# Performance work log

Measured on AMD Instinct MI355X. Metric: run time of the kernel, lower is better.

## Reference

```python
import jax, jax.numpy as jnp
import numpy as np

NUM_NODES = 100000
NUM_EDGES = 50000
NUM_CONN = 800000
IN_DIM = 256
HIDDEN = 128
EDGE_ATTR_DIM = 17
LN_EPS = 1e-5


def setup_inputs() -> dict:
    key = jax.random.key(0)
    k1, k2, k3, kw1, kb1, kg, kbeta, kw2, kb2 = jax.random.split(key, 9)
    node_features = jax.random.normal(k1, (NUM_NODES, IN_DIM), dtype=jnp.float32)
    nodes = jax.random.randint(k2, (NUM_CONN,), 0, NUM_NODES, dtype=jnp.int64)
    edges = jax.random.randint(k3, (NUM_CONN,), 0, NUM_EDGES, dtype=jnp.int64)
    hyperedge_index = jnp.stack([nodes, edges], axis=0)
    # MLP params (Linear(in,hid) -> LayerNorm -> ReLU -> Dropout(eval:identity) -> Linear(hid,out))
    W1 = jax.random.normal(kw1, (IN_DIM, HIDDEN), dtype=jnp.float32) * (1.0 / np.sqrt(IN_DIM))
    b1 = jax.random.normal(kb1, (HIDDEN,), dtype=jnp.float32) * 0.01
    ln_g = jnp.ones((HIDDEN,), dtype=jnp.float32)
    ln_b = jnp.zeros((HIDDEN,), dtype=jnp.float32)
    W2 = jax.random.normal(kw2, (HIDDEN, EDGE_ATTR_DIM), dtype=jnp.float32) * (1.0 / np.sqrt(HIDDEN))
    b2 = jax.random.normal(kb2, (EDGE_ATTR_DIM,), dtype=jnp.float32) * 0.01
    return {"node_features": node_features, "hyperedge_index": hyperedge_index,
            "W1": W1, "b1": b1, "ln_g": ln_g, "ln_b": ln_b, "W2": W2, "b2": b2}


def reference(node_features, hyperedge_index, W1, b1, ln_g, ln_b, W2, b2):
    nodes = hyperedge_index[0]
    edges = hyperedge_index[1]
    # indices are in-range by construction (torch valid_mask is all-True here)
    gathered = node_features[nodes]                         # [num_conn, in_dim]
    summed = jax.ops.segment_sum(gathered, edges, num_segments=NUM_EDGES)
    counts = jax.ops.segment_sum(jnp.ones(edges.shape, node_features.dtype), edges,
                                 num_segments=NUM_EDGES)
    edge_features = summed / jnp.clip(counts, 1.0)[:, None]  # mean aggregation
    # decoder MLP (dropout inactive in eval)
    h = edge_features @ W1 + b1
    mu = jnp.mean(h, axis=-1, keepdims=True)
    var = jnp.mean(jnp.square(h - mu), axis=-1, keepdims=True)
    h = (h - mu) * jax.lax.rsqrt(var + LN_EPS) * ln_g + ln_b
    h = jax.nn.relu(h)
    return h @ W2 + b2                                      # [num_edges, edge_attr_dim]
```

## Files before the change

kernel.cpp:

```cpp
#include <hip/hip_runtime.h>
#include <hip/hip_bf16.h>
#include <stdint.h>

#define NUM_NODES 100000
#define NUM_EDGES 50000
#define NUM_CONN  800000
#define IN_DIM    256
#define HIDDEN    128
#define EDGE_DIM  17
#define PAD       64
#define CSTRIDE   16

typedef __bf16 bf16x8 __attribute__((ext_vector_type(8)));
typedef float  f32x4  __attribute__((ext_vector_type(4)));


__global__ void prep_kernel(const float* __restrict__ W1, const float* __restrict__ W2,
                            __bf16* __restrict__ w1f, __bf16* __restrict__ w2f,
                            int* __restrict__ counts2) {
    int i = blockIdx.x * 256 + threadIdx.x;
    if (i < NUM_EDGES) {
        int4 z = {0, 0, 0, 0};
        int4* c4 = (int4*)(counts2 + (size_t)i * CSTRIDE);
        c4[0] = z; c4[1] = z; c4[2] = z; c4[3] = z;
    }
    if (i < 4096) {
        int lane = i & 63, t = (i >> 6) & 7, kc2 = i >> 9;
        int m = lane & 15, q = lane >> 4;
        int n = t * 16 + m;
        int kbase = kc2 * 32 + q * 8;
        __bf16* dst = w1f + (size_t)i * 8;
        #pragma unroll
        for (int ki = 0; ki < 8; ++ki)
            dst[ki] = (__bf16)W1[(size_t)(kbase + ki) * HIDDEN + n];
    } else if (i < 4608) {
        int f = i - 4096;
        int lane = f & 63, t = (f >> 6) & 1, ks = f >> 7;
        int m = lane & 15, q = lane >> 4;
        int n = t * 16 + m;
        int kbase = ks * 32 + q * 8;
        __bf16* dst = w2f + (size_t)f * 8;
        #pragma unroll
        for (int ki = 0; ki < 8; ++ki)
            dst[ki] = (n < EDGE_DIM) ? (__bf16)W2[(size_t)(kbase + ki) * EDGE_DIM + n]
                                     : (__bf16)0.0f;
    }
}

#define FRONT_BLOCKS 2346
__global__ __launch_bounds__(256, 4) void front_kernel(const int* __restrict__ idx,
        int stride, int* __restrict__ counts2, int* __restrict__ slots,
        const float* __restrict__ nf, const __bf16* __restrict__ w1f,
        __bf16* __restrict__ pbf) {
    __shared__ __align__(16) __bf16 lds_w[16384];
    const int nb = blockIdx.x / 3, r3 = blockIdx.x % 3;
    if (r3 == 1) {
        long c0 = ((long)nb * 256 + threadIdx.x) * 4;
        if (c0 < NUM_CONN) {
            int nd[4], ed[4];
            if (stride == 2) {
                #pragma unroll
                for (int k = 0; k < 2; ++k) {
                    int4 vn = ((const int4*)idx)[c0 / 2 + k];
                    int4 ve = ((const int4*)(idx + 2 * NUM_CONN))[c0 / 2 + k];
                    nd[2 * k] = vn.x; nd[2 * k + 1] = vn.z;
                    ed[2 * k] = ve.x; ed[2 * k + 1] = ve.z;
                }
            } else {
                #pragma unroll
                for (int k = 0; k < 4; ++k) {
                    nd[k] = idx[c0 + k];
                    ed[k] = idx[NUM_CONN + c0 + k];
                }
            }
            int pos[4];
            #pragma unroll
            for (int k = 0; k < 4; ++k)
                pos[k] = atomicAdd(&counts2[(size_t)ed[k] * CSTRIDE], 1);
            #pragma unroll
            for (int k = 0; k < 4; ++k)
                if (pos[k] < PAD) slots[(size_t)ed[k] * PAD + pos[k]] = nd[k];
        }
        return;
    }
    const int p = 2 * nb + (r3 == 2 ? 1 : 0);
    const int wave = threadIdx.x >> 6;
    const int lane = threadIdx.x & 63;
    const int m = lane & 15, q = lane >> 4;
    int row = p * 64 + wave * 16 + m;
    if (row >= NUM_NODES) row = NUM_NODES - 1;
    const float* ap = nf + (size_t)row * IN_DIM + q * 8;

    const uint4* src = (const uint4*)w1f;
    uint4* dst = (uint4*)lds_w;

    bf16x8 afr[8];
    {
        float4 a4[8];
        #pragma unroll
        for (int kc2 = 0; kc2 < 4; ++kc2) {
            a4[2 * kc2]     = *(const float4*)(ap + kc2 * 32);
            a4[2 * kc2 + 1] = *(const float4*)(ap + kc2 * 32 + 4);
        }
        #pragma unroll
        for (int i = threadIdx.x; i < 2048; i += 256) {
            int kc2 = i >> 8, tt = (i >> 6) & 3, l = i & 63;
            dst[i] = src[(kc2 * 8 + tt) * 64 + l];
        }
        #pragma unroll
        for (int kc2 = 0; kc2 < 4; ++kc2) {
            float4 f0 = a4[2 * kc2], f1 = a4[2 * kc2 + 1];
            afr[kc2][0] = (__bf16)f0.x; afr[kc2][1] = (__bf16)f0.y;
            afr[kc2][2] = (__bf16)f0.z; afr[kc2][3] = (__bf16)f0.w;
            afr[kc2][4] = (__bf16)f1.x; afr[kc2][5] = (__bf16)f1.y;
            afr[kc2][6] = (__bf16)f1.z; afr[kc2][7] = (__bf16)f1.w;
        }
        #pragma unroll
        for (int kc2 = 4; kc2 < 8; ++kc2) {
            a4[2 * (kc2 - 4)]     = *(const float4*)(ap + kc2 * 32);
            a4[2 * (kc2 - 4) + 1] = *(const float4*)(ap + kc2 * 32 + 4);
        }
        #pragma unroll
        for (int kc2 = 4; kc2 < 8; ++kc2) {
            float4 f0 = a4[2 * (kc2 - 4)], f1 = a4[2 * (kc2 - 4) + 1];
            afr[kc2][0] = (__bf16)f0.x; afr[kc2][1] = (__bf16)f0.y;
            afr[kc2][2] = (__bf16)f0.z; afr[kc2][3] = (__bf16)f0.w;
            afr[kc2][4] = (__bf16)f1.x; afr[kc2][5] = (__bf16)f1.y;
            afr[kc2][6] = (__bf16)f1.z; afr[kc2][7] = (__bf16)f1.w;
        }
    }
    __syncthreads();

    const bf16x8* frag = (const bf16x8*)lds_w;
    #pragma unroll
    for (int ph = 0; ph < 2; ++ph) {
        f32x4 acc[4];
        #pragma unroll
        for (int tt = 0; tt < 4; ++tt) acc[tt] = (f32x4){0.f, 0.f, 0.f, 0.f};
        #pragma unroll
        for (int kc2 = 0; kc2 < 8; ++kc2) {
            #pragma unroll
            for (int tt = 0; tt < 4; ++tt)
                acc[tt] = __builtin_amdgcn_mfma_f32_16x16x32_bf16(
                    afr[kc2], frag[(kc2 * 4 + tt) * 64 + lane], acc[tt], 0, 0, 0);
        }
        int ob = p * 64 + wave * 16 + q * 4;
        #pragma unroll
        for (int tt = 0; tt < 4; ++tt) {
            int col = (ph * 4 + tt) * 16 + m;
            #pragma unroll
            for (int r = 0; r < 4; ++r) {
                int orow = ob + r;
                if (orow < NUM_NODES)
                    pbf[(size_t)orow * HIDDEN + col] = (__bf16)acc[tt][r];
            }
        }
        if (ph == 0) {
            __syncthreads();
            #pragma unroll
            for (int i = threadIdx.x; i < 2048; i += 256) {
                int kc2 = i >> 8, tt = (i >> 6) & 3, l = i & 63;
                dst[i] = src[(kc2 * 8 + 4 + tt) * 64 + l];
            }
            __syncthreads();
        }
    }
}

__global__ __launch_bounds__(256) void edge_kernel(const uint4* __restrict__ p4,
        const int* __restrict__ counts2, const int* __restrict__ slots,
        const float* __restrict__ b1, const float* __restrict__ ln_g,
        const float* __restrict__ ln_b, const __bf16* __restrict__ w2f,
        const float* __restrict__ b2, float* __restrict__ out) {
    __shared__ __align__(16) uint4 lds_r[256];
    const int wave = threadIdx.x >> 6;
    const int lane = threadIdx.x & 63;
    const int g = lane & 15, ge = lane >> 4;
    const int el = wave * 4 + ge;
    const int e = blockIdx.x * 16 + el;

    const int c = counts2[(size_t)e * CSTRIDE];
    const int cc = c < PAD ? c : PAD;
    const float inv = 1.0f / (float)(c > 0 ? c : 1);

    float acc[8];
    #pragma unroll
    for (int d = 0; d < 8; ++d) acc[d] = 0.f;

    for (int c0 = 0; c0 < cc; c0 += 16) {
        int slv = slots[(size_t)e * PAD + c0 + g];
        int lim = cc - c0; if (lim > 16) lim = 16;
        if (lim == 16) {
            #pragma unroll
            for (int k0 = 0; k0 < 16; k0 += 8) {
                uint4 u[8];
                #pragma unroll
                for (int k = 0; k < 8; ++k) {
                    int nd = __shfl(slv, ge * 16 + k0 + k, 64);
                    u[k] = p4[(size_t)nd * 16 + g];
                }
                #pragma unroll
                for (int k = 0; k < 8; ++k) {
                    acc[0] += __uint_as_float(u[k].x << 16);
                    acc[1] += __uint_as_float(u[k].x & 0xffff0000u);
                    acc[2] += __uint_as_float(u[k].y << 16);
                    acc[3] += __uint_as_float(u[k].y & 0xffff0000u);
                    acc[4] += __uint_as_float(u[k].z << 16);
                    acc[5] += __uint_as_float(u[k].z & 0xffff0000u);
                    acc[6] += __uint_as_float(u[k].w << 16);
                    acc[7] += __uint_as_float(u[k].w & 0xffff0000u);
                }
            }
        } else {
            for (int k0 = 0; k0 < lim; k0 += 4) {
                uint4 u[4];
                unsigned okm[4];
                #pragma unroll
                for (int k = 0; k < 4; ++k) {
                    int nd = __shfl(slv, ge * 16 + k0 + k, 64);
                    nd = ((unsigned)nd < NUM_NODES) ? nd : 0;
                    u[k] = p4[(size_t)nd * 16 + g];
                    okm[k] = (k0 + k < lim) ? 0xffffffffu : 0u;
                }
                #pragma unroll
                for (int k = 0; k < 4; ++k) {
                    uint4 v = u[k];
                    v.x &= okm[k]; v.y &= okm[k]; v.z &= okm[k]; v.w &= okm[k];
                    acc[0] += __uint_as_float(v.x << 16);
                    acc[1] += __uint_as_float(v.x & 0xffff0000u);
                    acc[2] += __uint_as_float(v.y << 16);
                    acc[3] += __uint_as_float(v.y & 0xffff0000u);
                    acc[4] += __uint_as_float(v.z << 16);
                    acc[5] += __uint_as_float(v.z & 0xffff0000u);
                    acc[6] += __uint_as_float(v.w << 16);
                    acc[7] += __uint_as_float(v.w & 0xffff0000u);
                }
            }
        }
    }

    float4 bA = ((const float4*)b1)[2 * g];
    float4 bB = ((const float4*)b1)[2 * g + 1];
    float h[8];
    h[0] = acc[0] * inv + bA.x; h[1] = acc[1] * inv + bA.y;
    h[2] = acc[2] * inv + bA.z; h[3] = acc[3] * inv + bA.w;
    h[4] = acc[4] * inv + bB.x; h[5] = acc[5] * inv + bB.y;
    h[6] = acc[6] * inv + bB.z; h[7] = acc[7] * inv + bB.w;

    float s = 0.f;
    #pragma unroll
    for (int d = 0; d < 8; ++d) s += h[d];
    #pragma unroll
    for (int off = 8; off > 0; off >>= 1) s += __shfl_xor(s, off, 64);
    float mu = s * (1.0f / 128.0f);

    float dv[8], vv = 0.f;
    #pragma unroll
    for (int d = 0; d < 8; ++d) { dv[d] = h[d] - mu; vv += dv[d] * dv[d]; }
    #pragma unroll
    for (int off = 8; off > 0; off >>= 1) vv += __shfl_xor(vv, off, 64);
    float rs = rsqrtf(vv * (1.0f / 128.0f) + 1e-5f);

    float4 gA = ((const float4*)ln_g)[2 * g];
    float4 gB = ((const float4*)ln_g)[2 * g + 1];
    float4 eA = ((const float4*)ln_b)[2 * g];
    float4 eB = ((const float4*)ln_b)[2 * g + 1];
    float gg[8] = {gA.x, gA.y, gA.z, gA.w, gB.x, gB.y, gB.z, gB.w};
    float ee[8] = {eA.x, eA.y, eA.z, eA.w, eB.x, eB.y, eB.z, eB.w};
    union { __bf16 b[8]; uint4 u; } pk;
    #pragma unroll
    for (int d = 0; d < 8; ++d) {
        float r = dv[d] * rs * gg[d] + ee[d];
        pk.b[d] = (__bf16)(r > 0.f ? r : 0.f);
    }
    lds_r[el * 16 + g] = pk.u;
    __syncthreads();

    if (wave == 0) {
        const int m = lane & 15, q = lane >> 4;
        const __bf16* lr = (const __bf16*)lds_r;
        const bf16x8* fw = (const bf16x8*)w2f;
        f32x4 a0 = (f32x4){0.f, 0.f, 0.f, 0.f};
        f32x4 a1 = (f32x4){0.f, 0.f, 0.f, 0.f};
        #pragma unroll
        for (int ks = 0; ks < 4; ++ks) {
            bf16x8 a = *(const bf16x8*)(lr + m * 128 + ks * 32 + q * 8);
            a0 = __builtin_amdgcn_mfma_f32_16x16x32_bf16(a, fw[(ks * 2 + 0) * 64 + lane], a0, 0, 0, 0);
            a1 = __builtin_amdgcn_mfma_f32_16x16x32_bf16(a, fw[(ks * 2 + 1) * 64 + lane], a1, 0, 0, 0);
        }
        int rowb = blockIdx.x * 16 + q * 4;
        float bm = b2[m];
        float b16 = b2[16];
        #pragma unroll
        for (int r = 0; r < 4; ++r) {
            out[(size_t)(rowb + r) * EDGE_DIM + m] = a0[r] + bm;
            if (m == 0) out[(size_t)(rowb + r) * EDGE_DIM + 16] = a1[r] + b16;
        }
    }
}

extern "C" void kernel_launch(void* const* d_in, const int* in_sizes, int n_in,
                              void* d_out, int out_size, void* d_ws, size_t ws_size,
                              hipStream_t stream) {
    const float* nf  = (const float*)d_in[0];
    const int*   idx = (const int*)d_in[1];
    const float* W1  = (const float*)d_in[2];
    const float* b1  = (const float*)d_in[3];
    const float* g   = (const float*)d_in[4];
    const float* be  = (const float*)d_in[5];
    const float* W2  = (const float*)d_in[6];
    const float* b2  = (const float*)d_in[7];
    float* out = (float*)d_out;

    char* ws = (char*)d_ws;
    __bf16* P       = (__bf16*)ws;
    int*    counts2 = (int*)(ws + 25600000);
    int*    slots   = (int*)(ws + 28800000);
    __bf16* W1F     = (__bf16*)(ws + 41600000);
    __bf16* W2F     = (__bf16*)(ws + 41665536);

    int stride = (in_sizes[1] == 2 * NUM_CONN) ? 1 : 2;

    prep_kernel<<<196, 256, 0, stream>>>(W1, W2, W1F, W2F, counts2);
    front_kernel<<<FRONT_BLOCKS, 256, 0, stream>>>(idx, stride, counts2, slots, nf, W1F, P);
    edge_kernel<<<NUM_EDGES / 16, 256, 0, stream>>>((const uint4*)P, counts2, slots,
                                                    b1, g, be, W2F, b2, out);
}
```

Baseline: 235.4 us.

## Process eight edges per wave and run per-wave MFMA without block sync

Each wave now aggregates eight edges in two sequential passes and performs its own second-layer MFMA on its own LDS slice. The block-wide barrier is removed, and the MFMA stage no longer runs on a single wave. The grid halves to cover 32 edges per block. In exchange, half of each MFMA tile is wasted on unused rows, and there are fewer concurrent waves for latency hiding on the irregular gather.

```diff
diff --git a/kernel.cpp b/kernel.cpp
--- a/kernel.cpp
+++ b/kernel.cpp
@@ -167,134 +167,143 @@
     }
 }
 
+#define EDGE_BLOCKS 1563
 __global__ __launch_bounds__(256) void edge_kernel(const uint4* __restrict__ p4,
         const int* __restrict__ counts2, const int* __restrict__ slots,
         const float* __restrict__ b1, const float* __restrict__ ln_g,
         const float* __restrict__ ln_b, const __bf16* __restrict__ w2f,
         const float* __restrict__ b2, float* __restrict__ out) {
-    __shared__ __align__(16) uint4 lds_r[256];
+    __shared__ __align__(16) uint4 lds_r[1024];
     const int wave = threadIdx.x >> 6;
     const int lane = threadIdx.x & 63;
     const int g = lane & 15, ge = lane >> 4;
-    const int el = wave * 4 + ge;
-    const int e = blockIdx.x * 16 + el;
-
-    const int c = counts2[(size_t)e * CSTRIDE];
-    const int cc = c < PAD ? c : PAD;
-    const float inv = 1.0f / (float)(c > 0 ? c : 1);
-
-    float acc[8];
+
     #pragma unroll
-    for (int d = 0; d < 8; ++d) acc[d] = 0.f;
-
-    for (int c0 = 0; c0 < cc; c0 += 16) {
-        int slv = slots[(size_t)e * PAD + c0 + g];
-        int lim = cc - c0; if (lim > 16) lim = 16;
-        if (lim == 16) {
-            #pragma unroll
-            for (int k0 = 0; k0 < 16; k0 += 8) {
-                uint4 u[8];
+    for (int rr = 0; rr < 2; ++rr) {
+        const int le = rr * 4 + ge;
+        const int e = blockIdx.x * 32 + wave * 8 + le;
+
+        int c = 0;
+        if (e < NUM_EDGES) c = counts2[(size_t)e * CSTRIDE];
+        const int cc = c < PAD ? c : PAD;
+        const float inv = 1.0f / (float)(c > 0 ? c : 1);
+
+        float acc[8];
+        #pragma unroll
+        for (int d = 0; d < 8; ++d) acc[d] = 0.f;
+
+        for (int c0 = 0; c0 < cc; c0 += 16) {
+            int slv = slots[(size_t)e * PAD + c0 + g];
+            int lim = cc - c0; if (lim > 16) lim = 16;
+            if (lim == 16) {
                 #pragma unroll
-                for (int k = 0; k < 8; ++k) {
-                    int nd = __shfl(slv, ge * 16 + k0 + k, 64);
-                    u[k] = p4[(size_t)nd * 16 + g];
+                for (int k0 = 0; k0 < 16; k0 += 8) {
+                    uint4 u[8];
+                    #pragma unroll
+                    for (int k = 0; k < 8; ++k) {
+                        int nd = __shfl(slv, ge * 16 + k0 + k, 64);
+                        u[k] = p4[(size_t)nd * 16 + g];
+                    }
+                    #pragma unroll
+                    for (int k = 0; k < 8; ++k) {
+                        acc[0] += __uint_as_float(u[k].x << 16);
+                        acc[1] += __uint_as_float(u[k].x & 0xffff0000u);
+                        acc[2] += __uint_as_float(u[k].y << 16);
+                        acc[3] += __uint_as_float(u[k].y & 0xffff0000u);
+                        acc[4] += __uint_as_float(u[k].z << 16);
+                        acc[5] += __uint_as_float(u[k].z & 0xffff0000u);
+                        acc[6] += __uint_as_float(u[k].w << 16);
+                        acc[7] += __uint_as_float(u[k].w & 0xffff0000u);
+                    }
                 }
-                #pragma unroll
-                for (int k = 0; k < 8; ++k) {
-                    acc[0] += __uint_as_float(u[k].x << 16);
-                    acc[1] += __uint_as_float(u[k].x & 0xffff0000u);
-                    acc[2] += __uint_as_float(u[k].y << 16);
-                    acc[3] += __uint_as_float(u[k].y & 0xffff0000u);
-                    acc[4] += __uint_as_float(u[k].z << 16);
-                    acc[5] += __uint_as_float(u[k].z & 0xffff0000u);
-                    acc[6] += __uint_as_float(u[k].w << 16);
-                    acc[7] += __uint_as_float(u[k].w & 0xffff0000u);
+            } else {
+                for (int k0 = 0; k0 < lim; k0 += 4) {
+                    uint4 u[4];
+                    unsigned okm[4];
+                    #pragma unroll
+                    for (int k = 0; k < 4; ++k) {
+                        int nd = __shfl(slv, ge * 16 + k0 + k, 64);
+                        nd = ((unsigned)nd < NUM_NODES) ? nd : 0;
+                        u[k] = p4[(size_t)nd * 16 + g];
+                        okm[k] = (k0 + k < lim) ? 0xffffffffu : 0u;
+                    }
+                    #pragma unroll
+                    for (int k = 0; k < 4; ++k) {
+                        uint4 v = u[k];
+                        v.x &= okm[k]; v.y &= okm[k]; v.z &= okm[k]; v.w &= okm[k];
+                        acc[0] += __uint_as_float(v.x << 16);
+                        acc[1] += __uint_as_float(v.x & 0xffff0000u);
+                        acc[2] += __uint_as_float(v.y << 16);
+                        acc[3] += __uint_as_float(v.y & 0xffff0000u);
+                        acc[4] += __uint_as_float(v.z << 16);
+                        acc[5] += __uint_as_float(v.z & 0xffff0000u);
+                        acc[6] += __uint_as_float(v.w << 16);
+                        acc[7] += __uint_as_float(v.w & 0xffff0000u);
+                    }
                 }
             }
-        } else {
-            for (int k0 = 0; k0 < lim; k0 += 4) {
-                uint4 u[4];
-                unsigned okm[4];
-                #pragma unroll
-                for (int k = 0; k < 4; ++k) {
-                    int nd = __shfl(slv, ge * 16 + k0 + k, 64);
-                    nd = ((unsigned)nd < NUM_NODES) ? nd : 0;
-                    u[k] = p4[(size_t)nd * 16 + g];
-                    okm[k] = (k0 + k < lim) ? 0xffffffffu : 0u;
-                }
-                #pragma unroll
-                for (int k = 0; k < 4; ++k) {
-                    uint4 v = u[k];
-                    v.x &= okm[k]; v.y &= okm[k]; v.z &= okm[k]; v.w &= okm[k];
-                    acc[0] += __uint_as_float(v.x << 16);
-                    acc[1] += __uint_as_float(v.x & 0xffff0000u);
-                    acc[2] += __uint_as_float(v.y << 16);
-                    acc[3] += __uint_as_float(v.y & 0xffff0000u);
-                    acc[4] += __uint_as_float(v.z << 16);
-                    acc[5] += __uint_as_float(v.z & 0xffff0000u);
-                    acc[6] += __uint_as_float(v.w << 16);
-                    acc[7] += __uint_as_float(v.w & 0xffff0000u);
-                }
-            }
-        }
-    }
-
-    float4 bA = ((const float4*)b1)[2 * g];
-    float4 bB = ((const float4*)b1)[2 * g + 1];
-    float h[8];
-    h[0] = acc[0] * inv + bA.x; h[1] = acc[1] * inv + bA.y;
-    h[2] = acc[2] * inv + bA.z; h[3] = acc[3] * inv + bA.w;
-    h[4] = acc[4] * inv + bB.x; h[5] = acc[5] * inv + bB.y;
-    h[6] = acc[6] * inv + bB.z; h[7] = acc[7] * inv + bB.w;
-
-    float s = 0.f;
-    #pragma unroll
-    for (int d = 0; d < 8; ++d) s += h[d];
-    #pragma unroll
-    for (int off = 8; off > 0; off >>= 1) s += __shfl_xor(s, off, 64);
-    float mu = s * (1.0f / 128.0f);
-
-    float dv[8], vv = 0.f;
-    #pragma unroll
-    for (int d = 0; d < 8; ++d) { dv[d] = h[d] - mu; vv += dv[d] * dv[d]; }
-    #pragma unroll
-    for (int off = 8; off > 0; off >>= 1) vv += __shfl_xor(vv, off, 64);
-    float rs = rsqrtf(vv * (1.0f / 128.0f) + 1e-5f);
-
-    float4 gA = ((const float4*)ln_g)[2 * g];
-    float4 gB = ((const float4*)ln_g)[2 * g + 1];
-    float4 eA = ((const float4*)ln_b)[2 * g];
-    float4 eB = ((const float4*)ln_b)[2 * g + 1];
-    float gg[8] = {gA.x, gA.y, gA.z, gA.w, gB.x, gB.y, gB.z, gB.w};
-    float ee[8] = {eA.x, eA.y, eA.z, eA.w, eB.x, eB.y, eB.z, eB.w};
-    union { __bf16 b[8]; uint4 u; } pk;
-    #pragma unroll
-    for (int d = 0; d < 8; ++d) {
-        float r = dv[d] * rs * gg[d] + ee[d];
-        pk.b[d] = (__bf16)(r > 0.f ? r : 0.f);
-    }
-    lds_r[el * 16 + g] = pk.u;
-    __syncthreads();
-
-    if (wave == 0) {
-        const int m = lane & 15, q = lane >> 4;
-        const __bf16* lr = (const __bf16*)lds_r;
+        }
+
+        float4 bA = ((const float4*)b1)[2 * g];
+        float4 bB = ((const float4*)b1)[2 * g + 1];
+        float h[8];
+        h[0] = acc[0] * inv + bA.x; h[1] = acc[1] * inv + bA.y;
+        h[2] = acc[2] * inv + bA.z; h[3] = acc[3] * inv + bA.w;
+        h[4] = acc[4] * inv + bB.x; h[5] = acc[5] * inv + bB.y;
+        h[6] = acc[6] * inv + bB.z; h[7] = acc[7] * inv + bB.w;
+
+        float s = 0.f;
+        #pragma unroll
+        for (int d = 0; d < 8; ++d) s += h[d];
+        #pragma unroll
+        for (int off = 8; off > 0; off >>= 1) s += __shfl_xor(s, off, 64);
+        float mu = s * (1.0f / 128.0f);
+
+        float dv[8], vv = 0.f;
+        #pragma unroll
+        for (int d = 0; d < 8; ++d) { dv[d] = h[d] - mu; vv += dv[d] * dv[d]; }
+        #pragma unroll
+        for (int off = 8; off > 0; off >>= 1) vv += __shfl_xor(vv, off, 64);
+        float rs = rsqrtf(vv * (1.0f / 128.0f) + 1e-5f);
+
+        float4 gA = ((const float4*)ln_g)[2 * g];
+        float4 gB = ((const float4*)ln_g)[2 * g + 1];
+        float4 eA = ((const float4*)ln_b)[2 * g];
+        float4 eB = ((const float4*)ln_b)[2 * g + 1];
+        float gg[8] = {gA.x, gA.y, gA.z, gA.w, gB.x, gB.y, gB.z, gB.w};
+        float ee[8] = {eA.x, eA.y, eA.z, eA.w, eB.x, eB.y, eB.z, eB.w};
+        union { __bf16 b[8]; uint4 u; } pk;
+        #pragma unroll
+        for (int d = 0; d < 8; ++d) {
+            float r = dv[d] * rs * gg[d] + ee[d];
+            pk.b[d] = (__bf16)(r > 0.f ? r : 0.f);
+        }
+        lds_r[wave * 256 + le * 16 + g] = pk.u;
+    }
+
+    {
+        const int mm = lane & 15, qq = lane >> 4;
+        const __bf16* lr = (const __bf16*)(lds_r + wave * 256);
         const bf16x8* fw = (const bf16x8*)w2f;
         f32x4 a0 = (f32x4){0.f, 0.f, 0.f, 0.f};
         f32x4 a1 = (f32x4){0.f, 0.f, 0.f, 0.f};
         #pragma unroll
         for (int ks = 0; ks < 4; ++ks) {
-            bf16x8 a = *(const bf16x8*)(lr + m * 128 + ks * 32 + q * 8);
+            bf16x8 a = *(const bf16x8*)(lr + mm * 128 + ks * 32 + qq * 8);
             a0 = __builtin_amdgcn_mfma_f32_16x16x32_bf16(a, fw[(ks * 2 + 0) * 64 + lane], a0, 0, 0, 0);
             a1 = __builtin_amdgcn_mfma_f32_16x16x32_bf16(a, fw[(ks * 2 + 1) * 64 + lane], a1, 0, 0, 0);
         }
-        int rowb = blockIdx.x * 16 + q * 4;
-        float bm = b2[m];
-        float b16 = b2[16];
+        const int rowb = blockIdx.x * 32 + wave * 8;
+        float bm = b2[mm];
+        float b16v = b2[16];
         #pragma unroll
         for (int r = 0; r < 4; ++r) {
-            out[(size_t)(rowb + r) * EDGE_DIM + m] = a0[r] + bm;
-            if (m == 0) out[(size_t)(rowb + r) * EDGE_DIM + 16] = a1[r] + b16;
+            int lrow = qq * 4 + r;
+            int orow = rowb + lrow;
+            if (lrow < 8 && orow < NUM_EDGES) {
+                out[(size_t)orow * EDGE_DIM + mm] = a0[r] + bm;
+                if (mm == 0) out[(size_t)orow * EDGE_DIM + 16] = a1[r] + b16v;
+            }
         }
     }
 }
@@ -323,6 +332,6 @@
 
     prep_kernel<<<196, 256, 0, stream>>>(W1, W2, W1F, W2F, counts2);
     front_kernel<<<FRONT_BLOCKS, 256, 0, stream>>>(idx, stride, counts2, slots, nf, W1F, P);
-    edge_kernel<<<NUM_EDGES / 16, 256, 0, stream>>>((const uint4*)P, counts2, slots,
-                                                    b1, g, be, W2F, b2, out);
+    edge_kernel<<<EDGE_BLOCKS, 256, 0, stream>>>((const uint4*)P, counts2, slots,
+                                                 b1, g, be, W2F, b2, out);
 }
```

Result: slower. 244.3 us (+3.8%).
